# Kernel tuning notes

Measured on AMD Instinct MI355X. Metric: run time of the kernel, lower is better.

Reference implementation:

```python
import jax, jax.numpy as jnp
import numpy as np

L, B, T, N, M = 2, 32, 256, 1024, 1024  # layers, batch, time, input feat, hidden


def setup_inputs() -> dict:
    key = jax.random.key(0)
    ks = jax.random.split(key, 7)
    s = 0.02  # weight init scale
    return {
        "x": jax.random.normal(ks[0], (B, T, N), dtype=jnp.float32),
        "h": jax.random.normal(ks[1], (L, B, M), dtype=jnp.float32) * 0.1,
        "c": jax.random.normal(ks[2], (L, B, M), dtype=jnp.float32) * 0.1,
        "Wih": jax.random.normal(ks[3], (L, 4 * M, N), dtype=jnp.float32) * s,
        "Whh": jax.random.normal(ks[4], (L, 4 * M, M), dtype=jnp.float32) * s,
        "bih": jnp.zeros((L, 4 * M), dtype=jnp.float32),
        "bhh": jnp.zeros((L, 4 * M), dtype=jnp.float32),
    }


def _lstm_cell(x_t, h_t, c_t, Wih_l, Whh_l, b_l):
    # gates: [i | f | g | o], matching torch.nn.LSTMCell layout
    gates = x_t @ Wih_l.T + h_t @ Whh_l.T + b_l  # (B, 4M)
    i, f, g, o = jnp.split(gates, 4, axis=-1)
    i, f, o = jax.nn.sigmoid(i), jax.nn.sigmoid(f), jax.nn.sigmoid(o)
    c_new = f * c_t + i * jnp.tanh(g)
    h_new = o * jnp.tanh(c_new)
    return h_new, c_new


def reference(x, h, c, Wih, Whh, bih, bhh):
    b_sum = bih + bhh  # (L, 4M)

    def step(carry, x_t):
        h_cur, c_cur = carry  # each (L, B, M)
        hs, cs = [], []
        inp = x_t
        for l in range(L):  # small fixed layer loop
            h_l, c_l = _lstm_cell(inp, h_cur[l], c_cur[l], Wih[l], Whh[l], b_sum[l])
            hs.append(h_l)
            cs.append(c_l)
            inp = h_l
        return (jnp.stack(hs, 0), jnp.stack(cs, 0)), inp  # emit top-layer h

    (h_final, c_final), outs_tbm = jax.lax.scan(step, (h, c), jnp.swapaxes(x, 0, 1))
    outs = jnp.swapaxes(outs_tbm, 0, 1)  # (B, T, M)
    return outs, h_final, c_final
```

## Files before the change

kernel.cpp:

```cpp
#include <hip/hip_runtime.h>


typedef __bf16 bf16x8 __attribute__((ext_vector_type(8)));
typedef float  f32x4  __attribute__((ext_vector_type(4)));
typedef unsigned u32x4 __attribute__((ext_vector_type(4)));

__device__ __forceinline__ unsigned short f2bf(float f) {
    union { float f; unsigned u; } v; v.f = f;
    unsigned u = v.u;
    unsigned r = u + 0x7fffu + ((u >> 16) & 1u);
    return (unsigned short)(r >> 16);
}
__device__ __forceinline__ float sigmoidf_fast(float x) {
    return 1.0f / (1.0f + __expf(-x));
}
__device__ __forceinline__ float tanhf_fast(float x) {
    return 1.0f - 2.0f / (__expf(2.0f * x) + 1.0f);
}

__global__ void cvt_w_concat(const float* __restrict__ src,
                             unsigned short* __restrict__ dst, int off, int n4) {
    int i = blockIdx.x * blockDim.x + threadIdx.x;
    int stride = gridDim.x * blockDim.x;
    for (; i < n4; i += stride) {
        float4 v = ((const float4*)src)[i];
        ushort4 o;
        o.x = f2bf(v.x); o.y = f2bf(v.y); o.z = f2bf(v.z); o.w = f2bf(v.w);
        int row = i >> 8;
        int c4  = i & 255;
        *(ushort4*)&dst[(size_t)row * 2048 + off + c4 * 4] = o;
    }
}

__global__ void cvt_x_tiles(const float* __restrict__ x,
                            unsigned short* __restrict__ xT) {
    int t = blockIdx.x, tid = threadIdx.x;
    unsigned short* tile = xT + (size_t)t * 32768;
    for (int b = 0; b < 32; ++b) {
        float4 v = *(const float4*)&x[((size_t)b * 256 + t) * 1024 + tid * 4];
        ushort4 o;
        o.x = f2bf(v.x); o.y = f2bf(v.y); o.z = f2bf(v.z); o.w = f2bf(v.w);
        *(ushort4*)&tile[(tid >> 2) * 512 + b * 16 + (tid & 3) * 4] = o;
    }
}

__global__ void cvt_h0_tiles(const float* __restrict__ h0,
                             unsigned short* __restrict__ h0T) {
    int l = blockIdx.x, tid = threadIdx.x;
    unsigned short* tile = h0T + (size_t)l * 32768;
    for (int b = 0; b < 32; ++b) {
        float4 v = *(const float4*)&h0[((size_t)l * 32 + b) * 1024 + tid * 4];
        ushort4 o;
        o.x = f2bf(v.x); o.y = f2bf(v.y); o.z = f2bf(v.z); o.w = f2bf(v.w);
        *(ushort4*)&tile[(tid >> 2) * 512 + b * 16 + (tid & 3) * 4] = o;
    }
}

__global__ void out_transpose(const float* __restrict__ outT,
                              float* __restrict__ out) {
    int t = blockIdx.x, tid = threadIdx.x;
    const float* tile = outT + (size_t)t * 32768;
    for (int b = 0; b < 32; ++b) {
        float4 v = *(const float4*)&tile[(tid >> 2) * 512 + b * 16 + (tid & 3) * 4];
        *(float4*)&out[((size_t)b * 256 + t) * 1024 + tid * 4] = v;
    }
}

__device__ __forceinline__ void pollge(const unsigned* fp, unsigned tgt) {
    while (true) {
        unsigned v = __hip_atomic_load(fp, __ATOMIC_RELAXED,
                                       __HIP_MEMORY_SCOPE_AGENT);
        if (__all((int)(v >= tgt))) break;
        __builtin_amdgcn_s_sleep(1);
    }
}

#define STAGE_LOADS(FLAGS_STR) \
    _Pragma("unroll") \
    for (int si = 0; si < 16; si++) \
        asm volatile("global_load_dwordx4 %0, %1, off" FLAGS_STR \
                     : "=v"(hv[si]) : "v"(gp + si * 4096) : "memory");

__global__ __launch_bounds__(256, 1) void lstm_fused(
    const unsigned short* __restrict__ Wcat,
    const unsigned short* __restrict__ xT,
    unsigned short* __restrict__ seqT,
    const unsigned short* __restrict__ h0T,
    unsigned short* __restrict__ hparT,
    float* __restrict__ outT,
    const float* __restrict__ c0,
    const float* __restrict__ bih, const float* __restrict__ bhh,
    float* __restrict__ out, unsigned int* flags)
{
    __shared__ __align__(16) unsigned short buf[32][1024];
    __shared__ __align__(16) float gred[4][2][4][16][20];
    __shared__ __align__(16) unsigned short hout_bf[32][16];
    __shared__ __align__(16) float hout_f[32][16];

    const int tid  = threadIdx.x;
    const int lane = tid & 63;
    const int w    = tid >> 6;
    const int l    = blockIdx.x >> 6;
    const int bidl = blockIdx.x & 63;
    const int m0   = bidl * 16;
    const int n    = lane & 15;
    const int g    = lane >> 4;
    const int lk   = g * 8;
    const int nn7  = n & 7;

    bf16x8 wx[32], wh[32];
    const unsigned short* Wl = Wcat + (size_t)l * 4096 * 2048;
    #pragma unroll
    for (int ct = 0; ct < 4; ct++) {
        int vc = ct * 16 + n;
        size_t jrow = (size_t)((vc & 3) * 1024 + m0 + (vc >> 2));
        #pragma unroll
        for (int kc = 0; kc < 8; kc++) {
            wx[ct*8+kc] = *(const bf16x8*)&Wl[jrow*2048 +        w*256 + kc*32 + lk];
            wh[ct*8+kc] = *(const bf16x8*)&Wl[jrow*2048 + 1024 + w*256 + kc*32 + lk];
        }
    }

    const int eb = lane >> 1;
    const int q  = lane & 1;
    const int em = m0 + 4 * w + 2 * q;
    float bs0[4], bs1[4];
    #pragma unroll
    for (int gg = 0; gg < 4; gg++) {
        bs0[gg] = bih[l*4096 + gg*1024 + em]     + bhh[l*4096 + gg*1024 + em];
        bs1[gg] = bih[l*4096 + gg*1024 + em + 1] + bhh[l*4096 + gg*1024 + em + 1];
    }
    float2 creg = *(const float2*)&c0[(size_t)l * 32768 + eb * 1024 + em];
    float2 hlast = {0.f, 0.f};
    const int uh = eb >> 4, urow = eb & 15;

    char* const bufb = (char*)&buf[0][0];
    const int sb  = (tid >> 1) & 31;
    char* const stL = bufb + sb * 2048
                    + ((w * 32 + (tid & 1) * 16) ^ ((sb & 7) << 4));

    const int hb64 = (nn7 >> 2) * 64;
    const int gx16 = (g ^ (nn7 & 3)) * 16;
    const char* rA0 = bufb + n * 2048 + w * 512 + gx16 + hb64;
    const char* rA1 = bufb + n * 2048 + w * 512 + gx16 + (64 - hb64);
    const char* rB0 = rA0 + 16 * 2048;
    const char* rB1 = rA1 + 16 * 2048;

    f32x4 acc0[4] = {}, acc1[4] = {};

    auto stage = [&](const char* tb, bool byp) {
        u32x4 hv[16];
        const char* gp = tb + tid * 16;
        if (byp) { STAGE_LOADS(" sc0 sc1") }
        else     { STAGE_LOADS("") }
        asm volatile("s_waitcnt vmcnt(0)" ::: "memory");
        #pragma unroll
        for (int si = 0; si < 16; si++)
            *(u32x4*)(stL + si * 128) = hv[si];
    };

    auto gemm = [&](const bf16x8* wf) {
        #pragma unroll
        for (int kc2 = 0; kc2 < 4; kc2++) {
            bf16x8 a0 = *(const bf16x8*)(rA0 + kc2 * 128);
            bf16x8 a1 = *(const bf16x8*)(rB0 + kc2 * 128);
            #pragma unroll
            for (int ct = 0; ct < 4; ct++) {
                acc0[ct] = __builtin_amdgcn_mfma_f32_16x16x32_bf16(a0, wf[ct*8+2*kc2], acc0[ct], 0,0,0);
                acc1[ct] = __builtin_amdgcn_mfma_f32_16x16x32_bf16(a1, wf[ct*8+2*kc2], acc1[ct], 0,0,0);
            }
            bf16x8 b0 = *(const bf16x8*)(rA1 + kc2 * 128);
            bf16x8 b1 = *(const bf16x8*)(rB1 + kc2 * 128);
            #pragma unroll
            for (int ct = 0; ct < 4; ct++) {
                acc0[ct] = __builtin_amdgcn_mfma_f32_16x16x32_bf16(b0, wf[ct*8+2*kc2+1], acc0[ct], 0,0,0);
                acc1[ct] = __builtin_amdgcn_mfma_f32_16x16x32_bf16(b1, wf[ct*8+2*kc2+1], acc1[ct], 0,0,0);
            }
        }
    };

    if (l == 0) {
        stage((const char*)xT, false);
        __syncthreads();
        gemm(wx);
    }
    __syncthreads();

    const int lag = l * 2;
    #pragma unroll 1
    for (int s = 0; s < 258; s++) {
        const int  t   = s - lag;
        const bool act = (t >= 0) && (t < 256);

        if (act) {
            const char* hb = (t == 0)
                ? (const char*)(h0T + (size_t)l * 32768)
                : (l == 0 ? (const char*)(seqT + (size_t)(t - 1) * 32768)
                          : (const char*)(hparT + (size_t)((t - 1) & 1) * 32768));
            stage(hb, true);
            __syncthreads();
            gemm(wh);
            {
                int r0 = g * 4;
                #pragma unroll
                for (int ct = 0; ct < 4; ct++) {
                    *(f32x4*)&gred[w][0][ct][n][r0] = acc0[ct];
                    *(f32x4*)&gred[w][1][ct][n][r0] = acc1[ct];
                }
            }
            __syncthreads();
            float g8[8];
            #pragma unroll
            for (int j = 0; j < 8; j++) {
                g8[j] = (gred[0][uh][w][8*q+j][urow] + gred[1][uh][w][8*q+j][urow])
                      + (gred[2][uh][w][8*q+j][urow] + gred[3][uh][w][8*q+j][urow]);
            }
            float gi0 = g8[0] + bs0[0], gf0 = g8[1] + bs0[1];
            float gg0 = g8[2] + bs0[2], go0 = g8[3] + bs0[3];
            float gi1 = g8[4] + bs1[0], gf1 = g8[5] + bs1[1];
            float gg1 = g8[6] + bs1[2], go1 = g8[7] + bs1[3];

            float c0n = sigmoidf_fast(gf0) * creg.x + sigmoidf_fast(gi0) * tanhf_fast(gg0);
            float c1n = sigmoidf_fast(gf1) * creg.y + sigmoidf_fast(gi1) * tanhf_fast(gg1);
            float h0v = sigmoidf_fast(go0) * tanhf_fast(c0n);
            float h1v = sigmoidf_fast(go1) * tanhf_fast(c1n);
            creg.x = c0n; creg.y = c1n;
            hlast.x = h0v; hlast.y = h1v;

            unsigned hp = (unsigned)f2bf(h0v) | ((unsigned)f2bf(h1v) << 16);
            *(unsigned*)&hout_bf[eb][4*w + 2*q] = hp;
            if (l == 1) {
                float2 hv2 = {h0v, h1v};
                *(float2*)&hout_f[eb][4*w + 2*q] = hv2;
            }
            __syncthreads();
            if (tid < 64) {
                u32x4 v = *(const u32x4*)((const char*)&hout_bf[0][0] + tid * 16);
                const char* dp = (l == 0)
                    ? (const char*)(seqT  + (size_t)t * 32768)       + bidl * 1024 + tid * 16
                    : (const char*)(hparT + (size_t)(t & 1) * 32768) + bidl * 1024 + tid * 16;
                asm volatile("global_store_dwordx4 %0, %1, off sc0 sc1"
                             :: "v"(dp), "v"(v) : "memory");
                asm volatile("s_waitcnt vmcnt(0)" ::: "memory");
                if (tid == 0)
                    __hip_atomic_store(flags + l * 64 + bidl, (unsigned)(s + 1),
                                       __ATOMIC_RELAXED, __HIP_MEMORY_SCOPE_AGENT);
            } else if (l == 1 && tid < 192) {
                int u = tid - 64;
                f32x4 v = *(const f32x4*)((const char*)&hout_f[0][0] + u * 16);
                *(f32x4*)((char*)outT + (size_t)t * 131072 + bidl * 2048 + u * 16) = v;
            }
        } else if (tid == 0) {
            __hip_atomic_store(flags + l * 64 + bidl, (unsigned)(s + 1),
                               __ATOMIC_RELAXED, __HIP_MEMORY_SCOPE_AGENT);
        }

        const int  tn   = t + 1;
        const bool xact = (tn >= ((l == 0) ? 1 : 0)) && (tn <= 255);
        if (xact) {
            stage(l == 0 ? (const char*)(xT   + (size_t)tn * 32768)
                         : (const char*)(seqT + (size_t)tn * 32768), l == 1);
            __syncthreads();
            #pragma unroll
            for (int ct = 0; ct < 4; ct++) {
                acc0[ct] = (f32x4){0.f, 0.f, 0.f, 0.f};
                acc1[ct] = (f32x4){0.f, 0.f, 0.f, 0.f};
            }
            gemm(wx);
        }

        if (tid < 128) pollge(flags + tid, (unsigned)(s + 1));
        __syncthreads();
    }

    float* hF = out + (size_t)8192 * 1024 + (size_t)l * 32768;
    float* cF = out + (size_t)8192 * 1024 + 65536 + (size_t)l * 32768;
    float2 hf2 = {hlast.x, hlast.y};
    *(float2*)&hF[eb * 1024 + em] = hf2;
    float2 cf2 = {creg.x, creg.y};
    *(float2*)&cF[eb * 1024 + em] = cf2;
}

extern "C" void kernel_launch(void* const* d_in, const int* in_sizes, int n_in,
                              void* d_out, int out_size, void* d_ws, size_t ws_size,
                              hipStream_t stream)
{
    const float* x   = (const float*)d_in[0];
    const float* h0  = (const float*)d_in[1];
    const float* c0  = (const float*)d_in[2];
    const float* Wih = (const float*)d_in[3];
    const float* Whh = (const float*)d_in[4];
    const float* bih = (const float*)d_in[5];
    const float* bhh = (const float*)d_in[6];
    float* out = (float*)d_out;

    char* p = (char*)d_ws;
    unsigned short* xT    = (unsigned short*)p; p += (size_t)256 * 32768 * 2;
    unsigned short* seqT  = (unsigned short*)p; p += (size_t)256 * 32768 * 2;
    unsigned short* Wcat  = (unsigned short*)p; p += (size_t)2 * 4096 * 2048 * 2;
    unsigned short* h0T   = (unsigned short*)p; p += (size_t)2 * 32768 * 2;
    unsigned short* hparT = (unsigned short*)p; p += (size_t)2 * 32768 * 2;
    float*          outT  = (float*)p;          p += (size_t)256 * 32768 * 4;
    unsigned int*   flags = (unsigned int*)p;   p += 4096;

    hipMemsetAsync(flags, 0, 4096, stream);
    cvt_w_concat<<<1024, 256, 0, stream>>>(Wih, Wcat, 0,    2 * 4096 * 256);
    cvt_w_concat<<<1024, 256, 0, stream>>>(Whh, Wcat, 1024, 2 * 4096 * 256);
    cvt_x_tiles<<<256, 256, 0, stream>>>(x, xT);
    cvt_h0_tiles<<<2, 256, 0, stream>>>(h0, h0T);

    lstm_fused<<<128, 256, 0, stream>>>(Wcat, xT, seqT, h0T, hparT, outT,
                                        c0, bih, bhh, out, flags);

    out_transpose<<<256, 256, 0, stream>>>(outT, out);
}
```

Baseline: 1.449 ms.

## Move input-projection GEMM onto critical path overlapped with recurrent h loads

```diff
diff --git a/kernel.cpp b/kernel.cpp
--- a/kernel.cpp
+++ b/kernel.cpp
@@ -75,11 +75,11 @@
     }
 }
 
-#define STAGE_LOADS(FLAGS_STR) \
+#define STAGE_LOADS(PTR, ARR, FLAGS_STR) \
     _Pragma("unroll") \
     for (int si = 0; si < 16; si++) \
         asm volatile("global_load_dwordx4 %0, %1, off" FLAGS_STR \
-                     : "=v"(hv[si]) : "v"(gp + si * 4096) : "memory");
+                     : "=v"(ARR[si]) : "v"(PTR + si * 4096) : "memory");
 
 __global__ __launch_bounds__(256, 1) void lstm_fused(
     const unsigned short* __restrict__ Wcat,
@@ -92,8 +92,8 @@
     const float* __restrict__ bih, const float* __restrict__ bhh,
     float* __restrict__ out, unsigned int* flags)
 {
-    __shared__ __align__(16) unsigned short buf[32][1024];
-    __shared__ __align__(16) float gred[4][2][4][16][20];
+    __shared__ __align__(16) unsigned short bufH[32][1024];
+    __shared__ __align__(16) unsigned short bufX[32][1024];
     __shared__ __align__(16) unsigned short hout_bf[32][16];
     __shared__ __align__(16) float hout_f[32][16];
 
@@ -134,56 +134,57 @@
     float2 hlast = {0.f, 0.f};
     const int uh = eb >> 4, urow = eb & 15;
 
-    char* const bufb = (char*)&buf[0][0];
-    const int sb  = (tid >> 1) & 31;
-    char* const stL = bufb + sb * 2048
-                    + ((w * 32 + (tid & 1) * 16) ^ ((sb & 7) << 4));
+    char* const bH = (char*)&bufH[0][0];
+    char* const bX = (char*)&bufX[0][0];
+    const int sb = (tid >> 1) & 31;
+    const int stOff = sb * 2048 + ((w * 32 + (tid & 1) * 16) ^ ((sb & 7) << 4));
+
+    typedef float GredT[2][4][16][20];
+    GredT* gred = (GredT*)bH;
 
     const int hb64 = (nn7 >> 2) * 64;
     const int gx16 = (g ^ (nn7 & 3)) * 16;
-    const char* rA0 = bufb + n * 2048 + w * 512 + gx16 + hb64;
-    const char* rA1 = bufb + n * 2048 + w * 512 + gx16 + (64 - hb64);
-    const char* rB0 = rA0 + 16 * 2048;
-    const char* rB1 = rA1 + 16 * 2048;
+    const int rOffA0 = n * 2048 + w * 512 + gx16 + hb64;
+    const int rOffA1 = n * 2048 + w * 512 + gx16 + (64 - hb64);
 
     f32x4 acc0[4] = {}, acc1[4] = {};
 
-    auto stage = [&](const char* tb, bool byp) {
+    auto gemmbuf = [&](const char* base, const bf16x8* wf) {
+        const char* pA0 = base + rOffA0;
+        const char* pA1 = base + rOffA1;
+        const char* pB0 = pA0 + 16 * 2048;
+        const char* pB1 = pA1 + 16 * 2048;
+        #pragma unroll
+        for (int kc2 = 0; kc2 < 4; kc2++) {
+            bf16x8 a0 = *(const bf16x8*)(pA0 + kc2 * 128);
+            bf16x8 a1 = *(const bf16x8*)(pB0 + kc2 * 128);
+            #pragma unroll
+            for (int ct = 0; ct < 4; ct++) {
+                acc0[ct] = __builtin_amdgcn_mfma_f32_16x16x32_bf16(a0, wf[ct*8+2*kc2], acc0[ct], 0,0,0);
+                acc1[ct] = __builtin_amdgcn_mfma_f32_16x16x32_bf16(a1, wf[ct*8+2*kc2], acc1[ct], 0,0,0);
+            }
+            bf16x8 b0 = *(const bf16x8*)(pA1 + kc2 * 128);
+            bf16x8 b1 = *(const bf16x8*)(pB1 + kc2 * 128);
+            #pragma unroll
+            for (int ct = 0; ct < 4; ct++) {
+                acc0[ct] = __builtin_amdgcn_mfma_f32_16x16x32_bf16(b0, wf[ct*8+2*kc2+1], acc0[ct], 0,0,0);
+                acc1[ct] = __builtin_amdgcn_mfma_f32_16x16x32_bf16(b1, wf[ct*8+2*kc2+1], acc1[ct], 0,0,0);
+            }
+        }
+    };
+
+    auto stageX = [&](const char* tb, bool byp) {
         u32x4 hv[16];
         const char* gp = tb + tid * 16;
-        if (byp) { STAGE_LOADS(" sc0 sc1") }
-        else     { STAGE_LOADS("") }
+        if (byp) { STAGE_LOADS(gp, hv, " sc0 sc1") }
+        else     { STAGE_LOADS(gp, hv, "") }
         asm volatile("s_waitcnt vmcnt(0)" ::: "memory");
         #pragma unroll
         for (int si = 0; si < 16; si++)
-            *(u32x4*)(stL + si * 128) = hv[si];
+            *(u32x4*)(bX + stOff + si * 128) = hv[si];
     };
 
-    auto gemm = [&](const bf16x8* wf) {
-        #pragma unroll
-        for (int kc2 = 0; kc2 < 4; kc2++) {
-            bf16x8 a0 = *(const bf16x8*)(rA0 + kc2 * 128);
-            bf16x8 a1 = *(const bf16x8*)(rB0 + kc2 * 128);
-            #pragma unroll
-            for (int ct = 0; ct < 4; ct++) {
-                acc0[ct] = __builtin_amdgcn_mfma_f32_16x16x32_bf16(a0, wf[ct*8+2*kc2], acc0[ct], 0,0,0);
-                acc1[ct] = __builtin_amdgcn_mfma_f32_16x16x32_bf16(a1, wf[ct*8+2*kc2], acc1[ct], 0,0,0);
-            }
-            bf16x8 b0 = *(const bf16x8*)(rA1 + kc2 * 128);
-            bf16x8 b1 = *(const bf16x8*)(rB1 + kc2 * 128);
-            #pragma unroll
-            for (int ct = 0; ct < 4; ct++) {
-                acc0[ct] = __builtin_amdgcn_mfma_f32_16x16x32_bf16(b0, wf[ct*8+2*kc2+1], acc0[ct], 0,0,0);
-                acc1[ct] = __builtin_amdgcn_mfma_f32_16x16x32_bf16(b1, wf[ct*8+2*kc2+1], acc1[ct], 0,0,0);
-            }
-        }
-    };
-
-    if (l == 0) {
-        stage((const char*)xT, false);
-        __syncthreads();
-        gemm(wx);
-    }
+    if (l == 0) stageX((const char*)xT, false);
     __syncthreads();
 
     const int lag = l * 2;
@@ -193,13 +194,32 @@
         const bool act = (t >= 0) && (t < 256);
 
         if (act) {
-            const char* hb = (t == 0)
+            const char* hbase = (t == 0)
                 ? (const char*)(h0T + (size_t)l * 32768)
                 : (l == 0 ? (const char*)(seqT + (size_t)(t - 1) * 32768)
                           : (const char*)(hparT + (size_t)((t - 1) & 1) * 32768));
-            stage(hb, true);
+            u32x4 hv[16];
+            {
+                const char* gp = hbase + tid * 16;
+                STAGE_LOADS(gp, hv, " sc0 sc1")
+            }
+            __builtin_amdgcn_sched_barrier(0);
+
+            #pragma unroll
+            for (int ct = 0; ct < 4; ct++) {
+                acc0[ct] = (f32x4){0.f, 0.f, 0.f, 0.f};
+                acc1[ct] = (f32x4){0.f, 0.f, 0.f, 0.f};
+            }
+            gemmbuf(bX, wx);
+
+            asm volatile("s_waitcnt vmcnt(0)" ::: "memory");
+            __builtin_amdgcn_sched_barrier(0);
+            #pragma unroll
+            for (int si = 0; si < 16; si++)
+                *(u32x4*)(bH + stOff + si * 128) = hv[si];
             __syncthreads();
-            gemm(wh);
+            gemmbuf(bH, wh);
+            __syncthreads();
             {
                 int r0 = g * 4;
                 #pragma unroll
@@ -258,15 +278,8 @@
         const int  tn   = t + 1;
         const bool xact = (tn >= ((l == 0) ? 1 : 0)) && (tn <= 255);
         if (xact) {
-            stage(l == 0 ? (const char*)(xT   + (size_t)tn * 32768)
-                         : (const char*)(seqT + (size_t)tn * 32768), l == 1);
-            __syncthreads();
-            #pragma unroll
-            for (int ct = 0; ct < 4; ct++) {
-                acc0[ct] = (f32x4){0.f, 0.f, 0.f, 0.f};
-                acc1[ct] = (f32x4){0.f, 0.f, 0.f, 0.f};
-            }
-            gemm(wx);
+            stageX(l == 0 ? (const char*)(xT   + (size_t)tn * 32768)
+                          : (const char*)(seqT + (size_t)tn * 32768), l == 1);
         }
 
         if (tid < 128) pollge(flags + tid, (unsigned)(s + 1));
```

After: 1.569 ms. 8.3% more time.

## Fuse LDS staging with MFMA GEMM per wave and drop block barriers

Applied to the files above, without the earlier changes.

```diff
diff --git a/kernel.cpp b/kernel.cpp
--- a/kernel.cpp
+++ b/kernel.cpp
@@ -74,12 +74,6 @@
         __builtin_amdgcn_s_sleep(1);
     }
 }
-
-#define STAGE_LOADS(FLAGS_STR) \
-    _Pragma("unroll") \
-    for (int si = 0; si < 16; si++) \
-        asm volatile("global_load_dwordx4 %0, %1, off" FLAGS_STR \
-                     : "=v"(hv[si]) : "v"(gp + si * 4096) : "memory");
 
 __global__ __launch_bounds__(256, 1) void lstm_fused(
     const unsigned short* __restrict__ Wcat,
@@ -135,56 +129,64 @@
     const int uh = eb >> 4, urow = eb & 15;
 
     char* const bufb = (char*)&buf[0][0];
-    const int sb  = (tid >> 1) & 31;
-    char* const stL = bufb + sb * 2048
-                    + ((w * 32 + (tid & 1) * 16) ^ ((sb & 7) << 4));
+    const int sb     = lane >> 1;
+    const int halfk  = lane & 1;
+    const int srcOff = w * 16384 + sb * 32 + halfk * 16;
+    const int sbRow  = sb * 2048;
+    const int ldsCol = w * 512 + halfk * 16;
+    const int swz    = (sb & 7) << 4;
 
     const int hb64 = (nn7 >> 2) * 64;
     const int gx16 = (g ^ (nn7 & 3)) * 16;
-    const char* rA0 = bufb + n * 2048 + w * 512 + gx16 + hb64;
-    const char* rA1 = bufb + n * 2048 + w * 512 + gx16 + (64 - hb64);
-    const char* rB0 = rA0 + 16 * 2048;
-    const char* rB1 = rA1 + 16 * 2048;
+    const int rOffA0 = n * 2048 + w * 512 + gx16 + hb64;
+    const int rOffA1 = n * 2048 + w * 512 + gx16 + (64 - hb64);
 
     f32x4 acc0[4] = {}, acc1[4] = {};
 
-    auto stage = [&](const char* tb, bool byp) {
+    auto stage_gemm = [&](const char* tb, const bf16x8* wfv, bool byp) {
         u32x4 hv[16];
-        const char* gp = tb + tid * 16;
-        if (byp) { STAGE_LOADS(" sc0 sc1") }
-        else     { STAGE_LOADS("") }
-        asm volatile("s_waitcnt vmcnt(0)" ::: "memory");
-        #pragma unroll
-        for (int si = 0; si < 16; si++)
-            *(u32x4*)(stL + si * 128) = hv[si];
+        const char* gp = tb + srcOff;
+        if (byp) {
+            #pragma unroll
+            for (int si = 0; si < 16; si++)
+                asm volatile("global_load_dwordx4 %0, %1, off sc0 sc1"
+                             : "=v"(hv[si]) : "v"(gp + si * 1024) : "memory");
+        } else {
+            #pragma unroll
+            for (int si = 0; si < 16; si++)
+                asm volatile("global_load_dwordx4 %0, %1, off"
+                             : "=v"(hv[si]) : "v"(gp + si * 1024) : "memory");
+        }
+        const char* pA0 = bufb + rOffA0;
+        const char* pA1 = bufb + rOffA1;
+        const char* pB0 = pA0 + 16 * 2048;
+        const char* pB1 = pA1 + 16 * 2048;
+#define SGRP(G4, VM) \
+        asm volatile("s_waitcnt vmcnt(" VM ")" ::: "memory"); \
+        _Pragma("unroll") \
+        for (int si = 4*(G4); si < 4*(G4)+4; si++) \
+            *(u32x4*)(bufb + sbRow + ((ldsCol + si*32) ^ swz)) = hv[si]; \
+        { \
+            bf16x8 a0 = *(const bf16x8*)(pA0 + (G4)*128); \
+            bf16x8 a1 = *(const bf16x8*)(pB0 + (G4)*128); \
+            _Pragma("unroll") \
+            for (int ct = 0; ct < 4; ct++) { \
+                acc0[ct] = __builtin_amdgcn_mfma_f32_16x16x32_bf16(a0, wfv[ct*8+2*(G4)],   acc0[ct],0,0,0); \
+                acc1[ct] = __builtin_amdgcn_mfma_f32_16x16x32_bf16(a1, wfv[ct*8+2*(G4)],   acc1[ct],0,0,0); \
+            } \
+            bf16x8 b0 = *(const bf16x8*)(pA1 + (G4)*128); \
+            bf16x8 b1 = *(const bf16x8*)(pB1 + (G4)*128); \
+            _Pragma("unroll") \
+            for (int ct = 0; ct < 4; ct++) { \
+                acc0[ct] = __builtin_amdgcn_mfma_f32_16x16x32_bf16(b0, wfv[ct*8+2*(G4)+1], acc0[ct],0,0,0); \
+                acc1[ct] = __builtin_amdgcn_mfma_f32_16x16x32_bf16(b1, wfv[ct*8+2*(G4)+1], acc1[ct],0,0,0); \
+            } \
+        }
+        SGRP(0, "12") SGRP(1, "8") SGRP(2, "4") SGRP(3, "0")
+#undef SGRP
     };
 
-    auto gemm = [&](const bf16x8* wf) {
-        #pragma unroll
-        for (int kc2 = 0; kc2 < 4; kc2++) {
-            bf16x8 a0 = *(const bf16x8*)(rA0 + kc2 * 128);
-            bf16x8 a1 = *(const bf16x8*)(rB0 + kc2 * 128);
-            #pragma unroll
-            for (int ct = 0; ct < 4; ct++) {
-                acc0[ct] = __builtin_amdgcn_mfma_f32_16x16x32_bf16(a0, wf[ct*8+2*kc2], acc0[ct], 0,0,0);
-                acc1[ct] = __builtin_amdgcn_mfma_f32_16x16x32_bf16(a1, wf[ct*8+2*kc2], acc1[ct], 0,0,0);
-            }
-            bf16x8 b0 = *(const bf16x8*)(rA1 + kc2 * 128);
-            bf16x8 b1 = *(const bf16x8*)(rB1 + kc2 * 128);
-            #pragma unroll
-            for (int ct = 0; ct < 4; ct++) {
-                acc0[ct] = __builtin_amdgcn_mfma_f32_16x16x32_bf16(b0, wf[ct*8+2*kc2+1], acc0[ct], 0,0,0);
-                acc1[ct] = __builtin_amdgcn_mfma_f32_16x16x32_bf16(b1, wf[ct*8+2*kc2+1], acc1[ct], 0,0,0);
-            }
-        }
-    };
-
-    if (l == 0) {
-        stage((const char*)xT, false);
-        __syncthreads();
-        gemm(wx);
-    }
-    __syncthreads();
+    if (l == 0) stage_gemm((const char*)xT, wx, false);
 
     const int lag = l * 2;
     #pragma unroll 1
@@ -197,9 +199,8 @@
                 ? (const char*)(h0T + (size_t)l * 32768)
                 : (l == 0 ? (const char*)(seqT + (size_t)(t - 1) * 32768)
                           : (const char*)(hparT + (size_t)((t - 1) & 1) * 32768));
-            stage(hb, true);
-            __syncthreads();
-            gemm(wh);
+            stage_gemm(hb, wh, true);
+
             {
                 int r0 = g * 4;
                 #pragma unroll
@@ -258,15 +259,14 @@
         const int  tn   = t + 1;
         const bool xact = (tn >= ((l == 0) ? 1 : 0)) && (tn <= 255);
         if (xact) {
-            stage(l == 0 ? (const char*)(xT   + (size_t)tn * 32768)
-                         : (const char*)(seqT + (size_t)tn * 32768), l == 1);
-            __syncthreads();
             #pragma unroll
             for (int ct = 0; ct < 4; ct++) {
                 acc0[ct] = (f32x4){0.f, 0.f, 0.f, 0.f};
                 acc1[ct] = (f32x4){0.f, 0.f, 0.f, 0.f};
             }
-            gemm(wx);
+            stage_gemm(l == 0 ? (const char*)(xT   + (size_t)tn * 32768)
+                              : (const char*)(seqT + (size_t)tn * 32768),
+                       wx, l == 1);
         }
 
         if (tid < 128) pollge(flags + tid, (unsigned)(s + 1));
```

Result: faster. 1.321 ms (-8.8%).
